# Kernel tuning notes

Measured on AMD Instinct MI355X. Metric: run time of the kernel, lower is better.

Reference implementation:

```python
import jax, jax.numpy as jnp
import numpy as np

N = 524288   # tokens (accounts)
D = 9        # num_prop_size
E = 2        # expert_size
H = 128      # expert MLP hidden
M = 32       # moe_out
O = 2        # output_size
K = 1        # top-k
LOSS_COF = 0.01
EPS = 1e-10


def setup_inputs() -> dict:
    key = jax.random.key(0)
    ks = jax.random.split(key, 10)
    f32 = jnp.float32
    return {
        "num_prop": jax.random.normal(ks[0], (N, D), f32),
        "cat_prop": jax.random.normal(ks[1], (N, 3), f32),
        "w_gate": jax.random.normal(ks[2], (D, E), f32) * 0.1,
        "W1": jax.random.normal(ks[3], (E, D, H), f32) * 0.1,
        "b1": jax.random.normal(ks[4], (E, H), f32) * 0.01,
        "W2": jax.random.normal(ks[5], (E, H, M), f32) * 0.1,
        "b2": jax.random.normal(ks[6], (E, M), f32) * 0.01,
        "Wout": jax.random.normal(ks[7], (M, O), f32) * 0.1,
        "bout": jax.random.normal(ks[8], (O,), f32) * 0.01,
        "k": K,
    }


def _cv_squared(x):
    # torch: x.var() (unbiased) / (x.mean()**2 + eps)
    return jnp.var(x, ddof=1) / (jnp.mean(x) ** 2 + EPS)


def reference(num_prop, cat_prop, w_gate, W1, b1, W2, b2, Wout, bout, k):
    x = num_prop                                   # eval mode: dropout = identity
    n, e = x.shape[0], w_gate.shape[1]

    # --- top-k gating (eval: clean logits, no noise) ---
    logits = x @ w_gate                            # [N, E]
    top_logits, top_idx = jax.lax.top_k(logits, min(k + 1, e))
    top_k_gates = jax.nn.softmax(top_logits[:, :k], axis=1)   # [N, k]
    rows = jnp.arange(n)[:, None]
    gates = jnp.zeros_like(logits).at[rows, top_idx[:, :k]].set(top_k_gates)  # [N, E]

    importance = gates.sum(axis=0)                 # [E]
    load = (gates > 0).astype(jnp.float32).sum(axis=0)  # [E]
    loss = (_cv_squared(importance) + _cv_squared(load)) * LOSS_COF

    # --- experts: per-expert 2-layer MLP, computed dense (E=2) then gated combine ---
    h = jax.nn.relu(jnp.einsum("nd,edh->neh", x, W1) + b1)    # [N, E, H]
    y_e = jnp.einsum("neh,ehm->nem", h, W2) + b2              # [N, E, M]
    y = jnp.einsum("ne,nem->nm", gates, y_e)                  # [N, M]

    out = y @ Wout + bout                                     # [N, O]
    return (out, loss)
```

## Files before the change

kernel.cpp:

```cpp
#include <hip/hip_runtime.h>
#include <hip/hip_bf16.h>

#define NTOK 524288
#define TPB  256
#define NBLK (NTOK / TPB)

__device__ __forceinline__ float bf2f(unsigned short u) {
    union { unsigned int i; float f; } v;
    v.i = ((unsigned int)u) << 16;
    return v.f;
}

__device__ __forceinline__ float ldq(const void* p, int i, bool f32) {
    if (f32) return ((const float*)p)[i];
    return bf2f(((const unsigned short*)p)[i]);
}

__global__ void prep_kernel(const void* __restrict__ num_prop,
                            const void* __restrict__ wgate,
                            const void* __restrict__ W1,
                            const void* __restrict__ b1,
                            const void* __restrict__ W2,
                            const void* __restrict__ b2,
                            const void* __restrict__ Wout,
                            const void* __restrict__ bout,
                            unsigned int* __restrict__ cnt1,
                            int* __restrict__ flag,
                            float* __restrict__ bpp,
                            float* __restrict__ wgf,
                            float* __restrict__ wpack)
{
    __shared__ int sflag;
    const int t = threadIdx.x;
    if (t == 0) {
        const unsigned short* u = (const unsigned short*)num_prop;
        int f = 0;
        for (int i = 0; i < 72; ++i) {
            int e = (u[i] >> 7) & 0xFF;
            if (e < 64 || e > 191) f = 1;
        }
        sflag = f; *flag = f; *cnt1 = 0u;
    }
    __syncthreads();
    const bool f32 = (sflag != 0);

    if (t < 18) wgf[t] = ldq(wgate, t, f32);

    if (t < 4) {
        int e = t >> 1, o = t & 1;
        float acc = ldq(bout, o, f32);
        for (int m = 0; m < 32; ++m)
            acc += ldq(b2, e * 32 + m, f32) * ldq(Wout, m * 2 + o, f32);
        bpp[t] = acc;
    }

    const int e = t >> 7;
    const int j = t & 127;
    float p0 = 0.f, p1 = 0.f;
    for (int m = 0; m < 32; ++m) {
        float w = ldq(W2, (e * 128 + j) * 32 + m, f32);
        p0 += w * ldq(Wout, m * 2 + 0, f32);
        p1 += w * ldq(Wout, m * 2 + 1, f32);
    }
    float* dst = wpack + j * 24 + e * 12;
    #pragma unroll
    for (int d = 0; d < 9; ++d)
        dst[d] = ldq(W1, (e * 9 + d) * 128 + j, f32);
    dst[9]  = ldq(b1, e * 128 + j, f32);
    dst[10] = p0;
    dst[11] = p1;
}

__global__ __launch_bounds__(TPB, 8)
void moe_main(const void* __restrict__ xg,
              const int* __restrict__ flag,
              const float* __restrict__ wgf,
              const float* __restrict__ bpp,
              const float* __restrict__ wpack,
              unsigned int* __restrict__ cnt1,
              float2* __restrict__ out)
{
    __shared__ float xs[TPB * 9];
    __shared__ unsigned int cblk;
    const int tid = threadIdx.x;
    if (tid == 0) cblk = 0u;

    const bool f32 = (*flag) != 0;
    const int base = blockIdx.x * (TPB * 9);
    if (f32) {
        const float* xf = (const float*)xg;
        for (int i = tid; i < TPB * 9; i += TPB)
            xs[i] = xf[base + i];
    } else {
        const unsigned short* xu = (const unsigned short*)xg;
        for (int i = tid; i < TPB * 9; i += TPB)
            xs[i] = bf2f(xu[base + i]);
    }
    __syncthreads();

    float x[9];
    #pragma unroll
    for (int d = 0; d < 9; ++d) x[d] = xs[tid * 9 + d];

    float l0 = 0.f, l1 = 0.f;
    #pragma unroll
    for (int d = 0; d < 9; ++d) {
        l0 = fmaf(x[d], wgf[d * 2 + 0], l0);
        l1 = fmaf(x[d], wgf[d * 2 + 1], l1);
    }
    const bool e1 = l1 > l0;

    unsigned long long bal = __ballot(e1);
    if ((tid & 63) == 0)
        atomicAdd(&cblk, (unsigned int)__popcll(bal));

    float a00 = bpp[0], a01 = bpp[1], a10 = bpp[2], a11 = bpp[3];

    #pragma unroll 4
    for (int j = 0; j < 128; ++j) {
        const float* wp = wpack + j * 24;
        float h0 = wp[9], h1 = wp[21];
        #pragma unroll
        for (int d = 0; d < 9; ++d) {
            h0 = fmaf(x[d], wp[d],      h0);
            h1 = fmaf(x[d], wp[12 + d], h1);
        }
        h0 = fmaxf(h0, 0.f);
        h1 = fmaxf(h1, 0.f);
        a00 = fmaf(h0, wp[10], a00);
        a01 = fmaf(h0, wp[11], a01);
        a10 = fmaf(h1, wp[22], a10);
        a11 = fmaf(h1, wp[23], a11);
    }

    float2 o;
    o.x = e1 ? a10 : a00;
    o.y = e1 ? a11 : a01;
    out[blockIdx.x * TPB + tid] = o;

    __syncthreads();
    if (tid == 0) atomicAdd(cnt1, cblk);
}

__global__ void finalize_kernel(const unsigned int* __restrict__ cnt1,
                                float* __restrict__ loss_out)
{
    double c1 = (double)(*cnt1);
    double c0 = (double)NTOK - c1;
    double diff = c0 - c1;
    double mean = (double)NTOK * 0.5;
    double var  = 0.5 * diff * diff;
    double cv2  = var / (mean * mean + 1e-10);
    *loss_out = (float)(0.02 * cv2);
}

extern "C" void kernel_launch(void* const* d_in, const int* in_sizes, int n_in,
                              void* d_out, int out_size, void* d_ws, size_t ws_size,
                              hipStream_t stream) {
    const void* num_prop = d_in[0];
    const void* w_gate   = d_in[2];
    const void* W1       = d_in[3];
    const void* b1       = d_in[4];
    const void* W2       = d_in[5];
    const void* b2       = d_in[6];
    const void* Wout     = d_in[7];
    const void* bout     = d_in[8];

    char* ws = (char*)d_ws;
    unsigned int* cnt1 = (unsigned int*)ws;
    int* flag          = (int*)(ws + 8);
    float* bpp         = (float*)(ws + 16);
    float* wgf         = (float*)(ws + 64);
    float* wpack       = (float*)(ws + 192);

    float*  outf = (float*)d_out;
    float2* out2 = (float2*)d_out;

    hipLaunchKernelGGL(prep_kernel, dim3(1), dim3(256), 0, stream,
                       num_prop, w_gate, W1, b1, W2, b2, Wout, bout,
                       cnt1, flag, bpp, wgf, wpack);
    hipLaunchKernelGGL(moe_main, dim3(NBLK), dim3(TPB), 0, stream,
                       num_prop, flag, wgf, bpp, wpack, cnt1, out2);
    hipLaunchKernelGGL(finalize_kernel, dim3(1), dim3(1), 0, stream,
                       cnt1, outf + (size_t)NTOK * 2);
}
```

Before: 142.4 us.

## Sort tokens by expert within block to compute only selected expert per wave

Tokens in each block are partitioned by their gated expert using ballot and prefix counts, then permuted through shared memory, so most wavefronts evaluate only one expert MLP instead of both. A wave that straddles the expert boundary still computes both experts. The weight pack is relaid out per expert, results are scattered back to original order through shared memory, and the finalize kernel is folded into the main kernel with a last-block-done counter. This adds extra barriers and a permutation step but roughly halves the MLP arithmetic.

```diff
diff --git a/kernel.cpp b/kernel.cpp
--- a/kernel.cpp
+++ b/kernel.cpp
@@ -1,5 +1,4 @@
 #include <hip/hip_runtime.h>
-#include <hip/hip_bf16.h>
 
 #define NTOK 524288
 #define TPB  256
@@ -24,7 +23,7 @@
                             const void* __restrict__ b2,
                             const void* __restrict__ Wout,
                             const void* __restrict__ bout,
-                            unsigned int* __restrict__ cnt1,
+                            unsigned int* __restrict__ cnt_done,
                             int* __restrict__ flag,
                             float* __restrict__ bpp,
                             float* __restrict__ wgf,
@@ -39,7 +38,7 @@
             int e = (u[i] >> 7) & 0xFF;
             if (e < 64 || e > 191) f = 1;
         }
-        sflag = f; *flag = f; *cnt1 = 0u;
+        sflag = f; *flag = f; cnt_done[0] = 0u; cnt_done[1] = 0u;
     }
     __syncthreads();
     const bool f32 = (sflag != 0);
@@ -62,7 +61,7 @@
         p0 += w * ldq(Wout, m * 2 + 0, f32);
         p1 += w * ldq(Wout, m * 2 + 1, f32);
     }
-    float* dst = wpack + j * 24 + e * 12;
+    float* dst = wpack + e * 1536 + j * 12;
     #pragma unroll
     for (int d = 0; d < 9; ++d)
         dst[d] = ldq(W1, (e * 9 + d) * 128 + j, f32);
@@ -77,81 +76,124 @@
               const float* __restrict__ wgf,
               const float* __restrict__ bpp,
               const float* __restrict__ wpack,
-              unsigned int* __restrict__ cnt1,
-              float2* __restrict__ out)
+              unsigned int* __restrict__ cnt_done,
+              float2* __restrict__ out,
+              float* __restrict__ loss_out)
 {
     __shared__ float xs[TPB * 9];
-    __shared__ unsigned int cblk;
-    const int tid = threadIdx.x;
-    if (tid == 0) cblk = 0u;
+    __shared__ unsigned char smap[TPB];
+    __shared__ unsigned int wcnt[4];
+
+    const int tid  = threadIdx.x;
+    const int lane = tid & 63;
+    const int wave = tid >> 6;
 
     const bool f32 = (*flag) != 0;
-    const int base = blockIdx.x * (TPB * 9);
+    const int gbase = blockIdx.x * (TPB * 9);
     if (f32) {
         const float* xf = (const float*)xg;
-        for (int i = tid; i < TPB * 9; i += TPB)
-            xs[i] = xf[base + i];
+        #pragma unroll
+        for (int i = 0; i < 9; ++i)
+            xs[tid + i * TPB] = xf[gbase + tid + i * TPB];
     } else {
         const unsigned short* xu = (const unsigned short*)xg;
         for (int i = tid; i < TPB * 9; i += TPB)
-            xs[i] = bf2f(xu[base + i]);
-    }
-    __syncthreads();
-
+            xs[i] = bf2f(xu[gbase + i]);
+    }
+    __syncthreads();
+
+    float l0 = 0.f, l1 = 0.f;
+    #pragma unroll
+    for (int d = 0; d < 9; ++d) {
+        float xv = xs[tid * 9 + d];
+        l0 = fmaf(xv, wgf[d * 2 + 0], l0);
+        l1 = fmaf(xv, wgf[d * 2 + 1], l1);
+    }
+    const bool e1 = l1 > l0;
+
+    unsigned long long bal = __ballot(e1);
+    if (lane == 0) wcnt[wave] = (unsigned int)__popcll(bal);
+    __syncthreads();
+    int pre = 0, tot = 0;
+    #pragma unroll
+    for (int w = 0; w < 4; ++w) {
+        int c = (int)wcnt[w];
+        if (w < wave) pre += c;
+        tot += c;
+    }
+    const int n1 = tot;
+    const int n0 = TPB - n1;
+    const int p1 = pre + (int)__popcll(bal & ((1ull << lane) - 1ull));
+    const int slot = e1 ? (n0 + p1) : (tid - p1);
+    smap[slot] = (unsigned char)tid;
+    if (tid == 0) atomicAdd(&cnt_done[0], (unsigned int)n1);
+    __syncthreads();
+
+    const int t = (int)smap[tid];
     float x[9];
     #pragma unroll
-    for (int d = 0; d < 9; ++d) x[d] = xs[tid * 9 + d];
-
-    float l0 = 0.f, l1 = 0.f;
-    #pragma unroll
-    for (int d = 0; d < 9; ++d) {
-        l0 = fmaf(x[d], wgf[d * 2 + 0], l0);
-        l1 = fmaf(x[d], wgf[d * 2 + 1], l1);
-    }
-    const bool e1 = l1 > l0;
-
-    unsigned long long bal = __ballot(e1);
-    if ((tid & 63) == 0)
-        atomicAdd(&cblk, (unsigned int)__popcll(bal));
-
-    float a00 = bpp[0], a01 = bpp[1], a10 = bpp[2], a11 = bpp[3];
-
-    #pragma unroll 4
-    for (int j = 0; j < 128; ++j) {
-        const float* wp = wpack + j * 24;
-        float h0 = wp[9], h1 = wp[21];
-        #pragma unroll
-        for (int d = 0; d < 9; ++d) {
-            h0 = fmaf(x[d], wp[d],      h0);
-            h1 = fmaf(x[d], wp[12 + d], h1);
-        }
-        h0 = fmaxf(h0, 0.f);
-        h1 = fmaxf(h1, 0.f);
-        a00 = fmaf(h0, wp[10], a00);
-        a01 = fmaf(h0, wp[11], a01);
-        a10 = fmaf(h1, wp[22], a10);
-        a11 = fmaf(h1, wp[23], a11);
-    }
-
-    float2 o;
-    o.x = e1 ? a10 : a00;
-    o.y = e1 ? a11 : a01;
-    out[blockIdx.x * TPB + tid] = o;
-
-    __syncthreads();
-    if (tid == 0) atomicAdd(cnt1, cblk);
-}
-
-__global__ void finalize_kernel(const unsigned int* __restrict__ cnt1,
-                                float* __restrict__ loss_out)
-{
-    double c1 = (double)(*cnt1);
-    double c0 = (double)NTOK - c1;
-    double diff = c0 - c1;
-    double mean = (double)NTOK * 0.5;
-    double var  = 0.5 * diff * diff;
-    double cv2  = var / (mean * mean + 1e-10);
-    *loss_out = (float)(0.02 * cv2);
+    for (int d = 0; d < 9; ++d) x[d] = xs[t * 9 + d];
+
+    const int wbase = __builtin_amdgcn_readfirstlane(tid) & 192;
+    const int n0u   = __builtin_amdgcn_readfirstlane(n0);
+
+    float2 res;
+    if (n0u <= wbase || n0u >= wbase + 64) {
+        const int ew = (n0u <= wbase) ? 1 : 0;
+        const float* wp = wpack + ew * 1536;
+        float a0 = bpp[ew * 2 + 0], a1 = bpp[ew * 2 + 1];
+        #pragma unroll 4
+        for (int j = 0; j < 128; ++j) {
+            const float* r = wp + j * 12;
+            float h = r[9];
+            #pragma unroll
+            for (int d = 0; d < 9; ++d) h = fmaf(x[d], r[d], h);
+            h = fmaxf(h, 0.f);
+            a0 = fmaf(h, r[10], a0);
+            a1 = fmaf(h, r[11], a1);
+        }
+        res.x = a0; res.y = a1;
+    } else {
+        const bool em = (tid >= n0);
+        float a00 = bpp[0], a01 = bpp[1], a10 = bpp[2], a11 = bpp[3];
+        #pragma unroll 4
+        for (int j = 0; j < 128; ++j) {
+            const float* r0 = wpack + j * 12;
+            const float* r1 = wpack + 1536 + j * 12;
+            float h0 = r0[9], h1 = r1[9];
+            #pragma unroll
+            for (int d = 0; d < 9; ++d) {
+                h0 = fmaf(x[d], r0[d], h0);
+                h1 = fmaf(x[d], r1[d], h1);
+            }
+            h0 = fmaxf(h0, 0.f);
+            h1 = fmaxf(h1, 0.f);
+            a00 = fmaf(h0, r0[10], a00);
+            a01 = fmaf(h0, r0[11], a01);
+            a10 = fmaf(h1, r1[10], a10);
+            a11 = fmaf(h1, r1[11], a11);
+        }
+        res.x = em ? a10 : a00;
+        res.y = em ? a11 : a01;
+    }
+
+    __syncthreads();
+    ((float2*)xs)[t] = res;
+    __syncthreads();
+    out[blockIdx.x * TPB + tid] = ((float2*)xs)[tid];
+
+    if (tid == 0) {
+        __threadfence();
+        unsigned int old = atomicAdd(&cnt_done[1], 1u);
+        if (old == NBLK - 1) {
+            double c1   = (double)atomicAdd(&cnt_done[0], 0u);
+            double c0   = (double)NTOK - c1;
+            double diff = c0 - c1;
+            double mean = (double)NTOK * 0.5;
+            double cv2  = (0.5 * diff * diff) / (mean * mean + 1e-10);
+            *loss_out = (float)(0.02 * cv2);
+        }
+    }
 }
 
 extern "C" void kernel_launch(void* const* d_in, const int* in_sizes, int n_in,
@@ -167,7 +209,7 @@
     const void* bout     = d_in[8];
 
     char* ws = (char*)d_ws;
-    unsigned int* cnt1 = (unsigned int*)ws;
+    unsigned int* cnt_done = (unsigned int*)ws;
     int* flag          = (int*)(ws + 8);
     float* bpp         = (float*)(ws + 16);
     float* wgf         = (float*)(ws + 64);
@@ -178,9 +220,8 @@
 
     hipLaunchKernelGGL(prep_kernel, dim3(1), dim3(256), 0, stream,
                        num_prop, w_gate, W1, b1, W2, b2, Wout, bout,
-                       cnt1, flag, bpp, wgf, wpack);
+                       cnt_done, flag, bpp, wgf, wpack);
     hipLaunchKernelGGL(moe_main, dim3(NBLK), dim3(TPB), 0, stream,
-                       num_prop, flag, wgf, bpp, wpack, cnt1, out2);
-    hipLaunchKernelGGL(finalize_kernel, dim3(1), dim3(1), 0, stream,
-                       cnt1, outf + (size_t)NTOK * 2);
-}
+                       num_prop, flag, wgf, bpp, wpack, cnt_done, out2,
+                       outf + (size_t)NTOK * 2);
+}
```

Result: slower. 174.0 us (+22.2%).

## Sort tokens by expert within block so waves compute only one expert

Applied to the files above, without the earlier changes.

Each block now handles 512 tokens, two per thread, and uses ballot prefix sums to partition them by selected expert in shared memory. Waves whose token range falls entirely in one expert evaluate only that expert's MLP, which roughly halves the FMA work. Only the boundary wave computes both experts. Weights are repacked per expert, and outputs are scattered back through shared memory for coalesced stores. The cost is extra barriers, a shared-memory permutation, higher register pressure (launch bounds lowered to 6), and half as many blocks.

```diff
diff --git a/kernel.cpp b/kernel.cpp
--- a/kernel.cpp
+++ b/kernel.cpp
@@ -1,9 +1,9 @@
 #include <hip/hip_runtime.h>
-#include <hip/hip_bf16.h>
 
 #define NTOK 524288
 #define TPB  256
-#define NBLK (NTOK / TPB)
+#define TOKB 512
+#define NBLK (NTOK / TOKB)
 
 __device__ __forceinline__ float bf2f(unsigned short u) {
     union { unsigned int i; float f; } v;
@@ -62,7 +62,7 @@
         p0 += w * ldq(Wout, m * 2 + 0, f32);
         p1 += w * ldq(Wout, m * 2 + 1, f32);
     }
-    float* dst = wpack + j * 24 + e * 12;
+    float* dst = wpack + e * 1536 + j * 12;
     #pragma unroll
     for (int d = 0; d < 9; ++d)
         dst[d] = ldq(W1, (e * 9 + d) * 128 + j, f32);
@@ -71,7 +71,7 @@
     dst[11] = p1;
 }
 
-__global__ __launch_bounds__(TPB, 8)
+__global__ __launch_bounds__(TPB, 6)
 void moe_main(const void* __restrict__ xg,
               const int* __restrict__ flag,
               const float* __restrict__ wgf,
@@ -80,66 +80,126 @@
               unsigned int* __restrict__ cnt1,
               float2* __restrict__ out)
 {
-    __shared__ float xs[TPB * 9];
-    __shared__ unsigned int cblk;
-    const int tid = threadIdx.x;
-    if (tid == 0) cblk = 0u;
+    __shared__ __align__(16) float xs[TOKB * 9];
+    __shared__ unsigned short smap[TOKB];
+    __shared__ unsigned int wcnt[8];
+
+    const int tid  = threadIdx.x;
+    const int lane = tid & 63;
+    const int wave = tid >> 6;
 
     const bool f32 = (*flag) != 0;
-    const int base = blockIdx.x * (TPB * 9);
+    const int gbase = blockIdx.x * (TOKB * 9);
     if (f32) {
         const float* xf = (const float*)xg;
-        for (int i = tid; i < TPB * 9; i += TPB)
-            xs[i] = xf[base + i];
+        #pragma unroll
+        for (int i = 0; i < 18; ++i)
+            xs[tid + i * TPB] = xf[gbase + tid + i * TPB];
     } else {
         const unsigned short* xu = (const unsigned short*)xg;
-        for (int i = tid; i < TPB * 9; i += TPB)
-            xs[i] = bf2f(xu[base + i]);
-    }
-    __syncthreads();
-
-    float x[9];
-    #pragma unroll
-    for (int d = 0; d < 9; ++d) x[d] = xs[tid * 9 + d];
-
-    float l0 = 0.f, l1 = 0.f;
+        for (int i = tid; i < TOKB * 9; i += TPB)
+            xs[i] = bf2f(xu[gbase + i]);
+    }
+    __syncthreads();
+
+    float l0A = 0.f, l1A = 0.f, l0B = 0.f, l1B = 0.f;
     #pragma unroll
     for (int d = 0; d < 9; ++d) {
-        l0 = fmaf(x[d], wgf[d * 2 + 0], l0);
-        l1 = fmaf(x[d], wgf[d * 2 + 1], l1);
-    }
-    const bool e1 = l1 > l0;
-
-    unsigned long long bal = __ballot(e1);
-    if ((tid & 63) == 0)
-        atomicAdd(&cblk, (unsigned int)__popcll(bal));
-
-    float a00 = bpp[0], a01 = bpp[1], a10 = bpp[2], a11 = bpp[3];
-
-    #pragma unroll 4
-    for (int j = 0; j < 128; ++j) {
-        const float* wp = wpack + j * 24;
-        float h0 = wp[9], h1 = wp[21];
-        #pragma unroll
-        for (int d = 0; d < 9; ++d) {
-            h0 = fmaf(x[d], wp[d],      h0);
-            h1 = fmaf(x[d], wp[12 + d], h1);
+        const float wa = wgf[d * 2 + 0], wb = wgf[d * 2 + 1];
+        const float xA = xs[tid * 9 + d];
+        const float xB = xs[(tid + 256) * 9 + d];
+        l0A = fmaf(xA, wa, l0A); l1A = fmaf(xA, wb, l1A);
+        l0B = fmaf(xB, wa, l0B); l1B = fmaf(xB, wb, l1B);
+    }
+    const bool e1A = l1A > l0A;
+    const bool e1B = l1B > l0B;
+
+    unsigned long long balA = __ballot(e1A);
+    unsigned long long balB = __ballot(e1B);
+    if (lane == 0) {
+        wcnt[wave]     = (unsigned int)__popcll(balA);
+        wcnt[4 + wave] = (unsigned int)__popcll(balB);
+    }
+    __syncthreads();
+    int pres[8]; int run = 0;
+    #pragma unroll
+    for (int c = 0; c < 8; ++c) { pres[c] = run; run += (int)wcnt[c]; }
+    const int n1 = run;
+    const int n0 = TOKB - n1;
+    const unsigned long long below = (1ull << lane) - 1ull;
+    const int prA = pres[wave]     + (int)__popcll(balA & below);
+    const int prB = pres[4 + wave] + (int)__popcll(balB & below);
+    const int slotA = e1A ? (n0 + prA) : (tid - prA);
+    const int slotB = e1B ? (n0 + prB) : (tid + 256 - prB);
+    smap[slotA] = (unsigned short)tid;
+    smap[slotB] = (unsigned short)(tid + 256);
+    __syncthreads();
+
+    const int sA = tid * 2, sB = sA + 1;
+    const int tA = (int)smap[sA], tB = (int)smap[sB];
+    float xa[9], xb[9];
+    #pragma unroll
+    for (int d = 0; d < 9; ++d) { xa[d] = xs[tA * 9 + d]; xb[d] = xs[tB * 9 + d]; }
+
+    const int wbase = __builtin_amdgcn_readfirstlane(tid & 192) << 1;
+    const int n0u   = __builtin_amdgcn_readfirstlane(n0);
+
+    float2 ra, rb;
+    if (n0u <= wbase || n0u >= wbase + 128) {
+        const int ew = (n0u <= wbase) ? 1 : 0;
+        const float* wp = wpack + ew * 1536;
+        float a0 = bpp[ew * 2 + 0], a1 = bpp[ew * 2 + 1];
+        float c0 = a0, c1 = a1;
+        #pragma unroll 4
+        for (int j = 0; j < 128; ++j) {
+            const float* r = wp + j * 12;
+            float hA = r[9], hB = r[9];
+            #pragma unroll
+            for (int d = 0; d < 9; ++d) {
+                hA = fmaf(xa[d], r[d], hA);
+                hB = fmaf(xb[d], r[d], hB);
+            }
+            hA = fmaxf(hA, 0.f); hB = fmaxf(hB, 0.f);
+            a0 = fmaf(hA, r[10], a0); a1 = fmaf(hA, r[11], a1);
+            c0 = fmaf(hB, r[10], c0); c1 = fmaf(hB, r[11], c1);
         }
-        h0 = fmaxf(h0, 0.f);
-        h1 = fmaxf(h1, 0.f);
-        a00 = fmaf(h0, wp[10], a00);
-        a01 = fmaf(h0, wp[11], a01);
-        a10 = fmaf(h1, wp[22], a10);
-        a11 = fmaf(h1, wp[23], a11);
-    }
-
-    float2 o;
-    o.x = e1 ? a10 : a00;
-    o.y = e1 ? a11 : a01;
-    out[blockIdx.x * TPB + tid] = o;
-
-    __syncthreads();
-    if (tid == 0) atomicAdd(cnt1, cblk);
+        ra.x = a0; ra.y = a1; rb.x = c0; rb.y = c1;
+    } else {
+        const bool eA = (sA >= n0u), eB = (sB >= n0u);
+        float aA0 = bpp[0], aA1 = bpp[1], aA2 = bpp[2], aA3 = bpp[3];
+        float aB0 = bpp[0], aB1 = bpp[1], aB2 = bpp[2], aB3 = bpp[3];
+        #pragma unroll 2
+        for (int j = 0; j < 128; ++j) {
+            const float* r0 = wpack + j * 12;
+            const float* r1 = wpack + 1536 + j * 12;
+            float hA0 = r0[9], hA1 = r1[9], hB0 = r0[9], hB1 = r1[9];
+            #pragma unroll
+            for (int d = 0; d < 9; ++d) {
+                hA0 = fmaf(xa[d], r0[d], hA0);
+                hA1 = fmaf(xa[d], r1[d], hA1);
+                hB0 = fmaf(xb[d], r0[d], hB0);
+                hB1 = fmaf(xb[d], r1[d], hB1);
+            }
+            hA0 = fmaxf(hA0, 0.f); hA1 = fmaxf(hA1, 0.f);
+            hB0 = fmaxf(hB0, 0.f); hB1 = fmaxf(hB1, 0.f);
+            aA0 = fmaf(hA0, r0[10], aA0); aA1 = fmaf(hA0, r0[11], aA1);
+            aA2 = fmaf(hA1, r1[10], aA2); aA3 = fmaf(hA1, r1[11], aA3);
+            aB0 = fmaf(hB0, r0[10], aB0); aB1 = fmaf(hB0, r0[11], aB1);
+            aB2 = fmaf(hB1, r1[10], aB2); aB3 = fmaf(hB1, r1[11], aB3);
+        }
+        ra.x = eA ? aA2 : aA0; ra.y = eA ? aA3 : aA1;
+        rb.x = eB ? aB2 : aB0; rb.y = eB ? aB3 : aB1;
+    }
+
+    __syncthreads();
+    float2* ob = (float2*)xs;
+    ob[tA] = ra;
+    ob[tB] = rb;
+    __syncthreads();
+    const int obase = blockIdx.x * TOKB;
+    out[obase + tid]       = ob[tid];
+    out[obase + 256 + tid] = ob[256 + tid];
+    if (tid == 0) atomicAdd(cnt1, (unsigned int)n1);
 }
 
 __global__ void finalize_kernel(const unsigned int* __restrict__ cnt1,
```

Result: faster. 132.8 us (-6.7%).
